# Kernel tuning notes

Measured on AMD Instinct MI355X. Metric: run time of the kernel, lower is better.

## Reference

```python
import jax, jax.numpy as jnp
import numpy as np

N_NODES = 131072
N_EDGES = 262144
N_GRAPHS = 4096
EMB = 300
N_LAYER = 5
N_TASKS = 1
NUM_ATOM_TYPE = 120
NUM_CHIRALITY = 3
NUM_BOND_TYPE = 6   # includes self-loop type 4
NUM_BOND_DIR = 3
SELF_LOOP_TYPE = 4
BN_EPS = 1e-5


def setup_inputs() -> dict:
    key = jax.random.key(0)
    ks = jax.random.split(key, 20)
    x = jnp.stack([
        jax.random.randint(ks[0], (N_NODES,), 0, NUM_ATOM_TYPE, dtype=jnp.int32),
        jax.random.randint(ks[1], (N_NODES,), 0, NUM_CHIRALITY, dtype=jnp.int32),
    ], axis=1)
    edge_index = jax.random.randint(ks[2], (2, N_EDGES), 0, N_NODES, dtype=jnp.int32)
    edge_attr = jnp.stack([
        jax.random.randint(ks[3], (N_EDGES,), 0, 4, dtype=jnp.int32),
        jax.random.randint(ks[4], (N_EDGES,), 0, NUM_BOND_DIR, dtype=jnp.int32),
    ], axis=1)
    # sorted batch vector, every graph non-empty (32 nodes per graph)
    batch = jnp.repeat(jnp.arange(N_GRAPHS, dtype=jnp.int32), N_NODES // N_GRAPHS)
    s = 0.05
    params = {
        'atom_emb0': jax.random.normal(ks[5], (NUM_ATOM_TYPE, EMB), jnp.float32) * s,
        'atom_emb1': jax.random.normal(ks[6], (NUM_CHIRALITY, EMB), jnp.float32) * s,
        'bond_emb0': jax.random.normal(ks[7], (N_LAYER, NUM_BOND_TYPE, EMB), jnp.float32) * s,
        'bond_emb1': jax.random.normal(ks[8], (N_LAYER, NUM_BOND_DIR, EMB), jnp.float32) * s,
        'W1': jax.random.normal(ks[9], (N_LAYER, EMB, 2 * EMB), jnp.float32) * s,
        'b1': jnp.zeros((N_LAYER, 2 * EMB), jnp.float32),
        'W2': jax.random.normal(ks[10], (N_LAYER, 2 * EMB, EMB), jnp.float32) * s,
        'b2': jnp.zeros((N_LAYER, EMB), jnp.float32),
        'bn_gamma': jnp.ones((N_LAYER, EMB), jnp.float32),
        'bn_beta': jnp.zeros((N_LAYER, EMB), jnp.float32),
        'head_W1': jax.random.normal(ks[11], (EMB, EMB // 2), jnp.float32) * s,
        'head_b1': jnp.zeros((EMB // 2,), jnp.float32),
        'head_W2': jax.random.normal(ks[12], (EMB // 2, N_TASKS), jnp.float32) * s,
        'head_b2': jnp.zeros((N_TASKS,), jnp.float32),
    }
    return dict(x=x, edge_index=edge_index, edge_attr=edge_attr, batch=batch,
                num_graphs=N_GRAPHS, **params)


def _gnn_forward(x, edge_index, edge_attr, batch, num_graphs,
                 atom_emb0, atom_emb1, bond_emb0, bond_emb1,
                 W1, b1, W2, b2, bn_gamma, bn_beta,
                 head_W1, head_b1, head_W2, head_b2):
    n = x.shape[0]
    L = W1.shape[0]
    # add self loops with bond type SELF_LOOP_TYPE
    loop = jnp.arange(n, dtype=edge_index.dtype)
    src = jnp.concatenate([edge_index[0], loop])
    dst = jnp.concatenate([edge_index[1], loop])
    ea0 = jnp.concatenate([edge_attr[:, 0], jnp.full((n,), SELF_LOOP_TYPE, edge_attr.dtype)])
    ea1 = jnp.concatenate([edge_attr[:, 1], jnp.zeros((n,), edge_attr.dtype)])

    h = atom_emb0[x[:, 0]] + atom_emb1[x[:, 1]]  # [N, EMB]
    for l in range(L):
        e = bond_emb0[l][ea0] + bond_emb1[l][ea1]           # [E+N, EMB]
        msg = h[src] + e                                     # gather + add
        agg = jax.ops.segment_sum(msg, dst, num_segments=n)  # [N, EMB]
        hid = jax.nn.relu(agg @ W1[l] + b1[l])
        h2 = hid @ W2[l] + b2[l]
        # BatchNorm1d (training-mode batch stats)
        mean = jnp.mean(h2, axis=0)
        var = jnp.var(h2, axis=0)
        h2 = (h2 - mean) * jax.lax.rsqrt(var + BN_EPS) * bn_gamma[l] + bn_beta[l]
        h = h2 if l == L - 1 else jax.nn.relu(h2)
    # super_node_rep: last node of each graph (batch is sorted)
    last_idx = jax.ops.segment_max(jnp.arange(n), batch, num_segments=num_graphs)
    sup = h[last_idx]                                        # [G, EMB]
    out = jax.nn.elu(sup @ head_W1 + head_b1) @ head_W2 + head_b2
    return out                                               # [G, num_tasks]


def reference(x, edge_index, edge_attr, batch, num_graphs,
              atom_emb0, atom_emb1, bond_emb0, bond_emb1,
              W1, b1, W2, b2, bn_gamma, bn_beta,
              head_W1, head_b1, head_W2, head_b2):
    return _gnn_forward(x, edge_index, edge_attr, batch, num_graphs,
                        atom_emb0, atom_emb1, bond_emb0, bond_emb1,
                        W1, b1, W2, b2, bn_gamma, bn_beta,
                        head_W1, head_b1, head_W2, head_b2)
```

## Files before the change

kernel.cpp:

```cpp
#include <hip/hip_runtime.h>
#include <hip/hip_bf16.h>

#define NN 131072
#define NE 262144
#define NG 4096
#define EMB 300
#define HS 320
#define K1 320
#define N1 640
#define K2E 608
#define N2P 384
#define NLAYER 5
#define NRB (NN / 128)

typedef __attribute__((ext_vector_type(8))) short short8;
typedef __attribute__((ext_vector_type(4))) float f32x4;
typedef __attribute__((ext_vector_type(4))) unsigned short ushort4v;

__device__ __forceinline__ void gload_lds16(const void* g, void* l) {
  __builtin_amdgcn_global_load_lds((const __attribute__((address_space(1))) void*)g,
                                   (__attribute__((address_space(3))) void*)l, 16, 0, 0);
}
__device__ __forceinline__ float b2f(unsigned short u) {
  return __uint_as_float(((unsigned)u) << 16);
}
__device__ __forceinline__ unsigned short f2b(float x) {
  __hip_bfloat16 b = __float2bfloat16(x);
  return *(unsigned short*)&b;
}


__global__ void prep_w1(const float* __restrict__ W1, __hip_bfloat16* __restrict__ W1T) {
  int idx = blockIdx.x * 256 + threadIdx.x;
  if (idx >= NLAYER * N1 * K1) return;
  int l = idx / (N1 * K1); int r = idx % (N1 * K1);
  int n = r / K1; int k = r % K1;
  float v = (n < 600 && k < 300) ? W1[(size_t)(l * 300 + k) * 600 + n] : 0.f;
  W1T[idx] = __float2bfloat16(v);
}

__global__ void prep_w2(const float* __restrict__ W2, __hip_bfloat16* __restrict__ W2T) {
  int idx = blockIdx.x * 256 + threadIdx.x;
  if (idx >= NLAYER * N2P * N1) return;
  int l = idx / (N2P * N1); int r = idx % (N2P * N1);
  int n = r / N1; int k = r % N1;
  float v = (n < 300 && k < 600) ? W2[(size_t)(l * 600 + k) * 300 + n] : 0.f;
  W2T[idx] = __float2bfloat16(v);
}

__global__ void prep_bias(const float* __restrict__ b1, const float* __restrict__ b2,
                          float* __restrict__ b1p, float* __restrict__ b2p) {
  int idx = blockIdx.x * 256 + threadIdx.x;
  if (idx < NLAYER * N1) {
    int l = idx / N1, n = idx % N1;
    b1p[idx] = (n < 600) ? b1[l * 600 + n] : 0.f;
  } else {
    int k = idx - NLAYER * N1;
    if (k < NLAYER * N2P) {
      int l = k / N2P, n = k % N2P;
      b2p[k] = (n < 300) ? b2[l * 300 + n] : 0.f;
    }
  }
}

__global__ void prep_etab(const float* __restrict__ bond0, const float* __restrict__ bond1,
                          float* __restrict__ etabg) {
  int idx = blockIdx.x * 256 + threadIdx.x;
  if (idx >= NLAYER * 13 * HS) return;
  int l = idx / (13 * HS); int r = idx % (13 * HS);
  int c = r / HS; int ch = r % HS;
  float val = 0.f;
  if (ch < EMB) {
    int t0 = (c < 12) ? (c / 3) : 4;
    int t1 = (c < 12) ? (c % 3) : 0;
    val = bond0[(size_t)(l * 6 + t0) * EMB + ch] + bond1[(size_t)(l * 3 + t1) * EMB + ch];
  }
  etabg[idx] = val;
}

__global__ void init_h(const int* __restrict__ x, const float* __restrict__ ae0,
                       const float* __restrict__ ae1, __hip_bfloat16* __restrict__ h) {
  int v = blockIdx.x; int t = threadIdx.x;
  int x0 = x[2 * v], x1 = x[2 * v + 1];
  for (int c = t; c < HS; c += 256)
    h[(size_t)v * HS + c] = __float2bfloat16(c < EMB ? ae0[x0 * EMB + c] + ae1[x1 * EMB + c] : 0.f);
}


__global__ void count_edges(const int* __restrict__ ei, int* __restrict__ counts) {
  int j = blockIdx.x * 256 + threadIdx.x;
  if (j >= NE) return;
  atomicAdd(&counts[ei[NE + j]], 1);
}

__global__ void scan_block(const int* __restrict__ counts, int* __restrict__ indptr,
                           int* __restrict__ blockSums) {
  __shared__ int s[256];
  int b = blockIdx.x, t = threadIdx.x;
  int base = b * 1024 + t * 4;
  int4 c = *(const int4*)&counts[base];
  int tsum = c.x + c.y + c.z + c.w;
  s[t] = tsum;
  __syncthreads();
  for (int off = 1; off < 256; off <<= 1) {
    int v = (t >= off) ? s[t - off] : 0;
    __syncthreads();
    s[t] += v;
    __syncthreads();
  }
  int excl = (t == 0) ? 0 : s[t - 1];
  indptr[base + 0] = excl;
  indptr[base + 1] = excl + c.x;
  indptr[base + 2] = excl + c.x + c.y;
  indptr[base + 3] = excl + c.x + c.y + c.z;
  if (t == 255) blockSums[b] = s[255];
}

__global__ void scan_top(const int* __restrict__ blockSums, int* __restrict__ blockOff) {
  __shared__ int s[128];
  int t = threadIdx.x;
  s[t] = blockSums[t];
  __syncthreads();
  for (int off = 1; off < 128; off <<= 1) {
    int v = (t >= off) ? s[t - off] : 0;
    __syncthreads();
    s[t] += v;
    __syncthreads();
  }
  blockOff[t] = (t == 0) ? 0 : s[t - 1];
}

__global__ void scan_add(int* __restrict__ indptr, const int* __restrict__ blockOff) {
  int b = blockIdx.x, t = threadIdx.x;
  int off = blockOff[b];
  int base = b * 1024 + t * 4;
  indptr[base + 0] += off; indptr[base + 1] += off;
  indptr[base + 2] += off; indptr[base + 3] += off;
  if (b == 127 && t == 255) indptr[NN] = NE;
}

__global__ void scatter_edges(const int* __restrict__ ei, const int* __restrict__ ea,
                              int* __restrict__ cursor, int* __restrict__ epacked) {
  int j = blockIdx.x * 256 + threadIdx.x;
  if (j >= NE) return;
  int dst = ei[NE + j];
  int src = ei[j];
  int c = ea[2 * j] * 3 + ea[2 * j + 1];
  int pos = atomicAdd(&cursor[dst], 1);
  epacked[pos] = src | (c << 17);
}

__global__ void last_idx_kernel(const int* __restrict__ batch, int* __restrict__ lastidx) {
  int i = blockIdx.x * 256 + threadIdx.x;
  if (i >= NN) return;
  int b = batch[i];
  if (i == NN - 1 || batch[i + 1] != b) lastidx[b] = i;
}

template<int BN>
__global__ __launch_bounds__(1024)
void aggregate_kernel(const __hip_bfloat16* __restrict__ hg, const int* __restrict__ indptr,
                      const int* __restrict__ epacked, const float* __restrict__ etabg,
                      const float* __restrict__ bnsc, const float* __restrict__ bnsh,
                      __hip_bfloat16* __restrict__ agg) {
  __shared__ float etab[13 * HS];
  const int tid = threadIdx.x;
#pragma unroll
  for (int idx = tid; idx < 13 * HS; idx += 1024)
    etab[idx] = etabg[idx];
  __syncthreads();
  const int wid = tid >> 6, lane = tid & 63;
  const int cA = lane * 4, cB = 256 + lane;
  const unsigned short* h = (const unsigned short*)hg;

  f32x4 scA = {1.f, 1.f, 1.f, 1.f}, shA = {0.f, 0.f, 0.f, 0.f};
  float scB = 1.f, shB = 0.f;
  if (BN) {
    scA = *(const f32x4*)&bnsc[cA]; shA = *(const f32x4*)&bnsh[cA];
    scB = bnsc[cB]; shB = bnsh[cB];
  }
  auto trA = [&](float x, int k) -> float {
    if (BN) x = fmaxf(fmaf(x, scA[k], shA[k]), 0.f);
    return x;
  };
  auto trB = [&](float x) -> float {
    if (BN) x = fmaxf(fmaf(x, scB, shB), 0.f);
    return x;
  };
  const float* es = etab + 12 * HS;

  for (int it = 0; it < 4; ++it) {
    const int v = blockIdx.x * 64 + it * 16 + wid;
    const unsigned short* hv = h + (size_t)v * HS;
    ushort4v pA = *(const ushort4v*)(hv + cA);
    unsigned short pB = hv[cB];
    float a0 = trA(b2f(pA[0]), 0) + es[cA];
    float a1 = trA(b2f(pA[1]), 1) + es[cA + 1];
    float a2 = trA(b2f(pA[2]), 2) + es[cA + 2];
    float a3 = trA(b2f(pA[3]), 3) + es[cA + 3];
    float a4 = trB(b2f(pB)) + es[cB];

    const int jb = indptr[v], je = indptr[v + 1];
    int j = jb;
    for (; j + 2 <= je; j += 2) {
      int p0 = epacked[j], p1 = epacked[j + 1];
      const unsigned short* h0 = h + (size_t)(p0 & (NN - 1)) * HS;
      const unsigned short* h1 = h + (size_t)(p1 & (NN - 1)) * HS;
      ushort4v q0 = *(const ushort4v*)(h0 + cA);
      ushort4v q1 = *(const ushort4v*)(h1 + cA);
      unsigned short r0 = h0[cB], r1 = h1[cB];
      const float* e0 = etab + (p0 >> 17) * HS;
      const float* e1 = etab + (p1 >> 17) * HS;
      a0 += trA(b2f(q0[0]), 0) + e0[cA]     + trA(b2f(q1[0]), 0) + e1[cA];
      a1 += trA(b2f(q0[1]), 1) + e0[cA + 1] + trA(b2f(q1[1]), 1) + e1[cA + 1];
      a2 += trA(b2f(q0[2]), 2) + e0[cA + 2] + trA(b2f(q1[2]), 2) + e1[cA + 2];
      a3 += trA(b2f(q0[3]), 3) + e0[cA + 3] + trA(b2f(q1[3]), 3) + e1[cA + 3];
      a4 += trB(b2f(r0)) + e0[cB] + trB(b2f(r1)) + e1[cB];
    }
    if (j < je) {
      int p0 = epacked[j];
      const unsigned short* h0 = h + (size_t)(p0 & (NN - 1)) * HS;
      ushort4v q0 = *(const ushort4v*)(h0 + cA);
      unsigned short r0 = h0[cB];
      const float* e0 = etab + (p0 >> 17) * HS;
      a0 += trA(b2f(q0[0]), 0) + e0[cA];
      a1 += trA(b2f(q0[1]), 1) + e0[cA + 1];
      a2 += trA(b2f(q0[2]), 2) + e0[cA + 2];
      a3 += trA(b2f(q0[3]), 3) + e0[cA + 3];
      a4 += trB(b2f(r0)) + e0[cB];
    }

    unsigned short* av = (unsigned short*)agg + (size_t)v * HS;
    ushort4v o; o[0] = f2b(a0); o[1] = f2b(a1); o[2] = f2b(a2); o[3] = f2b(a3);
    *(ushort4v*)(av + cA) = o;
    av[cB] = f2b(a4);
  }
}

template<int RELU, int STATS, int NBN, int KSTRIDE, int KEXT>
__global__ __launch_bounds__(256)
void gemm_kernel(const short* __restrict__ A, const short* __restrict__ BT,
                 const float* __restrict__ bias, __hip_bfloat16* __restrict__ Cout,
                 float* __restrict__ part, int outStride, int outBound, int rbBase) {
  __shared__ short smem[3 * 8192];
  __shared__ float sred[STATS ? 128 : 1][2];
  const int tid = threadIdx.x;
  const int wid = tid >> 6, lane = tid & 63;
  const int wm = wid >> 1, wn = wid & 1;
  f32x4 acc[4][4] = {};

  const int cpx = gridDim.x >> 3;
  const int logical = (blockIdx.x & 7) * cpx + (blockIdx.x >> 3);
  const int bn = logical % NBN;
  const int bm = logical / NBN;

  const short* Ag = A + (size_t)bm * 128 * KSTRIDE;
  const short* Bg = BT + (size_t)bn * 128 * KSTRIDE;
  const int r2 = tid >> 2;
  const int ksw = ((tid & 3) ^ ((tid >> 3) & 3)) * 8;
  const int arow_h = lane & 15;
  const int koffR = (((lane >> 4) ^ ((arow_h >> 1) & 3)) * 8);

  const short* Ao = Ag + (size_t)r2 * KSTRIDE + ksw;
  const short* Bo = Bg + (size_t)r2 * KSTRIDE + ksw;

  auto stage = [&](int buf, int kt) {
    short* s = smem + buf * 8192;
    gload_lds16(Ao + kt,                 s + tid * 8);
    gload_lds16(Ao + kt + 64 * KSTRIDE,  s + 2048 + tid * 8);
    gload_lds16(Bo + kt,                 s + 4096 + tid * 8);
    gload_lds16(Bo + kt + 64 * KSTRIDE,  s + 6144 + tid * 8);
  };

  constexpr int NT = KEXT / 32;
  stage(0, 0);
  stage(1, 32);
#pragma unroll
  for (int t = 0; t < NT; ++t) {
    if (t + 1 < NT) asm volatile("s_waitcnt vmcnt(4)" ::: "memory");
    else            asm volatile("s_waitcnt vmcnt(0)" ::: "memory");
    __builtin_amdgcn_sched_barrier(0);
    __builtin_amdgcn_s_barrier();
    const int rb = t % 3;
    if (t + 2 < NT) stage((t + 2) % 3, (t + 2) * 32);
    const short* sA = smem + rb * 8192 + wm * 2048;
    const short* sB = smem + rb * 8192 + 4096 + wn * 2048;
    short8 af[4], bf[4];
#pragma unroll
    for (int i = 0; i < 4; i++) af[i] = *(const short8*)&sA[(arow_h + i * 16) * 32 + koffR];
#pragma unroll
    for (int j = 0; j < 4; j++) bf[j] = *(const short8*)&sB[(arow_h + j * 16) * 32 + koffR];
#pragma unroll
    for (int i = 0; i < 4; i++)
#pragma unroll
      for (int j = 0; j < 4; j++)
        acc[i][j] = __builtin_amdgcn_mfma_f32_16x16x32_bf16(af[i], bf[j], acc[i][j], 0, 0, 0);
    __builtin_amdgcn_sched_barrier(0);
  }

  const int row0 = bm * 128 + wm * 64 + (lane >> 4) * 4;
  const int col0 = bn * 128 + wn * 64 + (lane & 15);
  float bs[4];
#pragma unroll
  for (int j = 0; j < 4; j++) bs[j] = bias[col0 + j * 16];
  float ssum[4] = {0, 0, 0, 0}, ssq[4] = {0, 0, 0, 0};
  if (STATS) {
    if (tid < 128) { sred[tid][0] = 0.f; sred[tid][1] = 0.f; }
    __syncthreads();
  }
#pragma unroll
  for (int i = 0; i < 4; i++) {
#pragma unroll
    for (int p = 0; p < 4; p++) {
      const size_t row = row0 + i * 16 + p;
#pragma unroll
      for (int j = 0; j < 4; j++) {
        const int col = col0 + j * 16;
        float v = acc[i][j][p] + bs[j];
        if (STATS) { ssum[j] += v; ssq[j] += v * v; }
        if (RELU) v = fmaxf(v, 0.f);
        if (col < outBound)
          Cout[row * (size_t)outStride + col] = __float2bfloat16(v);
      }
    }
  }
  if (STATS) {
#pragma unroll
    for (int j = 0; j < 4; j++) {
      const int cw = wn * 64 + j * 16 + (lane & 15);
      atomicAdd(&sred[cw][0], ssum[j]);
      atomicAdd(&sred[cw][1], ssq[j]);
    }
    __syncthreads();
    if (tid < 128) {
      const int col = bn * 128 + tid;
      if (col < EMB) {
        const int rb2 = rbBase + bm;
        part[(size_t)col * (2 * NRB) + rb2] = sred[tid][0];
        part[(size_t)col * (2 * NRB) + NRB + rb2] = sred[tid][1];
      }
    }
  }
}

__global__ __launch_bounds__(256)
void bn_finalize(const float* __restrict__ part, const float* __restrict__ gamma,
                 const float* __restrict__ beta, float* __restrict__ bnsc,
                 float* __restrict__ bnsh) {
  __shared__ float rs[256], rq[256];
  const int c = blockIdx.x, t = threadIdx.x;
  if (c >= EMB) {
    if (t == 0) { bnsc[c] = 0.f; bnsh[c] = 0.f; }
    return;
  }
  float s = 0.f, q = 0.f;
  for (int rb = t; rb < NRB; rb += 256) {
    s += part[(size_t)c * (2 * NRB) + rb];
    q += part[(size_t)c * (2 * NRB) + NRB + rb];
  }
  rs[t] = s; rq[t] = q;
  __syncthreads();
  for (int off = 128; off > 0; off >>= 1) {
    if (t < off) { rs[t] += rs[t + off]; rq[t] += rq[t + off]; }
    __syncthreads();
  }
  if (t == 0) {
    float mean = rs[0] / (float)NN;
    float var = rq[0] / (float)NN - mean * mean;
    float sc = rsqrtf(var + 1e-5f) * gamma[c];
    bnsc[c] = sc;
    bnsh[c] = beta[c] - mean * sc;
  }
}

__global__ __launch_bounds__(256)
void head_kernel(const __hip_bfloat16* __restrict__ h, const int* __restrict__ lastidx,
                 const float* __restrict__ bnsc4, const float* __restrict__ bnsh4,
                 const float* __restrict__ hW1, const float* __restrict__ hb1,
                 const float* __restrict__ hW2, const float* __restrict__ hb2,
                 float* __restrict__ out) {
  __shared__ float sup[EMB];
  __shared__ float red[256];
  int g = blockIdx.x, t = threadIdx.x;
  int v = lastidx[g];
  for (int c = t; c < EMB; c += 256)
    sup[c] = b2f(((const unsigned short*)h)[(size_t)v * HS + c]) * bnsc4[c] + bnsh4[c];
  __syncthreads();
  float val = 0.f;
  if (t < 150) {
    float acc = hb1[t];
    for (int k = 0; k < EMB; k++) acc += sup[k] * hW1[k * 150 + t];
    float e = (acc > 0.f) ? acc : (expf(acc) - 1.f);
    val = e * hW2[t];
  }
  red[t] = val;
  __syncthreads();
  for (int off = 128; off > 0; off >>= 1) {
    if (t < off) red[t] += red[t + off];
    __syncthreads();
  }
  if (t == 0) out[g] = red[0] + hb2[0];
}


extern "C" void kernel_launch(void* const* d_in, const int* in_sizes, int n_in,
                              void* d_out, int out_size, void* d_ws, size_t ws_size,
                              hipStream_t stream) {
  const int* x      = (const int*)d_in[0];
  const int* ei     = (const int*)d_in[1];
  const int* ea     = (const int*)d_in[2];
  const int* batch  = (const int*)d_in[3];
  const float* atom0 = (const float*)d_in[5];
  const float* atom1 = (const float*)d_in[6];
  const float* bond0 = (const float*)d_in[7];
  const float* bond1 = (const float*)d_in[8];
  const float* W1    = (const float*)d_in[9];
  const float* b1    = (const float*)d_in[10];
  const float* W2    = (const float*)d_in[11];
  const float* b2    = (const float*)d_in[12];
  const float* gamma = (const float*)d_in[13];
  const float* beta  = (const float*)d_in[14];
  const float* hW1   = (const float*)d_in[15];
  const float* hb1   = (const float*)d_in[16];
  const float* hW2   = (const float*)d_in[17];
  const float* hb2   = (const float*)d_in[18];
  float* out = (float*)d_out;

  char* p = (char*)d_ws;
  auto carve = [&](size_t b) -> void* {
    void* r = (void*)p;
    p += (b + 255) & ~(size_t)255;
    return r;
  };
  __hip_bfloat16* agg = (__hip_bfloat16*)carve((size_t)NN * HS * 2);
  __hip_bfloat16* h   = (__hip_bfloat16*)carve((size_t)NN * HS * 2);
  __hip_bfloat16* W1T = (__hip_bfloat16*)carve((size_t)NLAYER * N1 * K1 * 2);
  __hip_bfloat16* W2T = (__hip_bfloat16*)carve((size_t)NLAYER * N2P * N1 * 2);
  float* b1p          = (float*)carve((size_t)NLAYER * N1 * 4);
  float* b2p          = (float*)carve((size_t)NLAYER * N2P * 4);
  float* etabg        = (float*)carve((size_t)NLAYER * 13 * HS * 4);
  float* part         = (float*)carve((size_t)EMB * 2 * NRB * 4);
  float* bnsc         = (float*)carve((size_t)NLAYER * HS * 4);
  float* bnsh         = (float*)carve((size_t)NLAYER * HS * 4);
  int* counts         = (int*)carve((size_t)NN * 4);
  int* indptr         = (int*)carve((size_t)(NN + 1) * 4);
  int* cursor         = (int*)carve((size_t)NN * 4);
  int* epacked        = (int*)carve((size_t)NE * 4);
  int* blockSums      = (int*)carve(128 * 4);
  int* blockOff       = (int*)carve(128 * 4);
  int* lastidx        = (int*)carve((size_t)NG * 4);

  size_t used = (size_t)(p - (char*)d_ws);
  size_t avail = (ws_size > used + 4096) ? (ws_size - used - 4096) : 0;
  int CHUNK = 16384;
  if (avail >= (size_t)65536 * N1 * 2) CHUNK = 65536;
  else if (avail >= (size_t)32768 * N1 * 2) CHUNK = 32768;
  __hip_bfloat16* hid = (__hip_bfloat16*)carve((size_t)CHUNK * N1 * 2);

  hipMemsetAsync(counts, 0, (size_t)NN * 4, stream);

  prep_w1<<<(NLAYER * N1 * K1 + 255) / 256, 256, 0, stream>>>(W1, W1T);
  prep_w2<<<(NLAYER * N2P * N1 + 255) / 256, 256, 0, stream>>>(W2, W2T);
  prep_bias<<<(NLAYER * (N1 + N2P) + 255) / 256, 256, 0, stream>>>(b1, b2, b1p, b2p);
  prep_etab<<<(NLAYER * 13 * HS + 255) / 256, 256, 0, stream>>>(bond0, bond1, etabg);
  init_h<<<NN, 256, 0, stream>>>(x, atom0, atom1, h);

  count_edges<<<NE / 256, 256, 0, stream>>>(ei, counts);
  scan_block<<<128, 256, 0, stream>>>(counts, indptr, blockSums);
  scan_top<<<1, 128, 0, stream>>>(blockSums, blockOff);
  scan_add<<<128, 256, 0, stream>>>(indptr, blockOff);
  hipMemcpyAsync(cursor, indptr, (size_t)NN * 4, hipMemcpyDeviceToDevice, stream);
  scatter_edges<<<NE / 256, 256, 0, stream>>>(ei, ea, cursor, epacked);
  last_idx_kernel<<<NN / 256, 256, 0, stream>>>(batch, lastidx);

  for (int l = 0; l < NLAYER; l++) {
    if (l == 0)
      aggregate_kernel<0><<<NN / 64, 1024, 0, stream>>>(
          h, indptr, epacked, etabg + (size_t)l * 13 * HS, nullptr, nullptr, agg);
    else
      aggregate_kernel<1><<<NN / 64, 1024, 0, stream>>>(
          h, indptr, epacked, etabg + (size_t)l * 13 * HS,
          bnsc + (size_t)(l - 1) * HS, bnsh + (size_t)(l - 1) * HS, agg);
    for (int c0 = 0; c0 < NN; c0 += CHUNK) {
      gemm_kernel<1, 0, N1 / 128, K1, K1><<<(CHUNK / 128) * (N1 / 128), 256, 0, stream>>>(
          (const short*)(agg + (size_t)c0 * HS),
          (const short*)(W1T + (size_t)l * N1 * K1), b1p + l * N1,
          hid, nullptr, N1, N1, 0);
      gemm_kernel<0, 1, N2P / 128, N1, K2E><<<(CHUNK / 128) * (N2P / 128), 256, 0, stream>>>(
          (const short*)hid,
          (const short*)(W2T + (size_t)l * N2P * N1), b2p + l * N2P,
          h + (size_t)c0 * HS, part, HS, HS, c0 / 128);
    }
    bn_finalize<<<HS, 256, 0, stream>>>(part, gamma + (size_t)l * EMB, beta + (size_t)l * EMB,
                                        bnsc + (size_t)l * HS, bnsh + (size_t)l * HS);
  }

  head_kernel<<<NG, 256, 0, stream>>>(h, lastidx, bnsc + 4 * HS, bnsh + 4 * HS,
                                      hW1, hb1, hW2, hb2, out);
}
```

Before: 1.655 ms.

## Process two M-tiles per GEMM block with a continuous cross-tile load pipeline

Each GEMM workgroup now computes CH=2 consecutive 128-row output tiles for the same column tile. The triple-buffered global-to-LDS prefetch runs across the tile boundary, so loads for the next tile overlap the previous tile's epilogue and the pipeline prologue is paid once per block. The grid shrinks by half, and the BN stats reduction now uses explicit barriers per tile. In exchange there are fewer blocks, which may lower occupancy or load balance, and the epilogue is serialized with the next tile's compute.

```diff
diff --git a/kernel.cpp b/kernel.cpp
--- a/kernel.cpp
+++ b/kernel.cpp
@@ -12,6 +12,7 @@
 #define N2P 384
 #define NLAYER 5
 #define NRB (NN / 128)
+#define CH 2
 
 typedef __attribute__((ext_vector_type(8))) short short8;
 typedef __attribute__((ext_vector_type(4))) float f32x4;
@@ -247,14 +248,13 @@
   const int tid = threadIdx.x;
   const int wid = tid >> 6, lane = tid & 63;
   const int wm = wid >> 1, wn = wid & 1;
-  f32x4 acc[4][4] = {};
 
   const int cpx = gridDim.x >> 3;
   const int logical = (blockIdx.x & 7) * cpx + (blockIdx.x >> 3);
   const int bn = logical % NBN;
-  const int bm = logical / NBN;
-
-  const short* Ag = A + (size_t)bm * 128 * KSTRIDE;
+  const int chain = logical / NBN;
+
+  const short* Ag = A + (size_t)(chain * CH) * 128 * KSTRIDE;
   const short* Bg = BT + (size_t)bn * 128 * KSTRIDE;
   const int r2 = tid >> 2;
   const int ksw = ((tid & 3) ^ ((tid >> 3) & 3)) * 8;
@@ -264,81 +264,93 @@
   const short* Ao = Ag + (size_t)r2 * KSTRIDE + ksw;
   const short* Bo = Bg + (size_t)r2 * KSTRIDE + ksw;
 
-  auto stage = [&](int buf, int kt) {
-    short* s = smem + buf * 8192;
-    gload_lds16(Ao + kt,                 s + tid * 8);
-    gload_lds16(Ao + kt + 64 * KSTRIDE,  s + 2048 + tid * 8);
-    gload_lds16(Bo + kt,                 s + 4096 + tid * 8);
-    gload_lds16(Bo + kt + 64 * KSTRIDE,  s + 6144 + tid * 8);
+  constexpr int NT = KEXT / 32;
+  constexpr int GT = NT * CH;
+
+  auto stage = [&](int g) {
+    const int mt = g / NT;
+    const int kt = (g % NT) * 32;
+    short* s = smem + (g % 3) * 8192;
+    gload_lds16(Ao + mt * 128 * KSTRIDE + kt,                s + tid * 8);
+    gload_lds16(Ao + mt * 128 * KSTRIDE + kt + 64 * KSTRIDE, s + 2048 + tid * 8);
+    gload_lds16(Bo + kt,                                     s + 4096 + tid * 8);
+    gload_lds16(Bo + kt + 64 * KSTRIDE,                      s + 6144 + tid * 8);
   };
 
-  constexpr int NT = KEXT / 32;
-  stage(0, 0);
-  stage(1, 32);
-#pragma unroll
-  for (int t = 0; t < NT; ++t) {
-    if (t + 1 < NT) asm volatile("s_waitcnt vmcnt(4)" ::: "memory");
-    else            asm volatile("s_waitcnt vmcnt(0)" ::: "memory");
-    __builtin_amdgcn_sched_barrier(0);
-    __builtin_amdgcn_s_barrier();
-    const int rb = t % 3;
-    if (t + 2 < NT) stage((t + 2) % 3, (t + 2) * 32);
-    const short* sA = smem + rb * 8192 + wm * 2048;
-    const short* sB = smem + rb * 8192 + 4096 + wn * 2048;
-    short8 af[4], bf[4];
-#pragma unroll
-    for (int i = 0; i < 4; i++) af[i] = *(const short8*)&sA[(arow_h + i * 16) * 32 + koffR];
-#pragma unroll
-    for (int j = 0; j < 4; j++) bf[j] = *(const short8*)&sB[(arow_h + j * 16) * 32 + koffR];
-#pragma unroll
-    for (int i = 0; i < 4; i++)
-#pragma unroll
-      for (int j = 0; j < 4; j++)
-        acc[i][j] = __builtin_amdgcn_mfma_f32_16x16x32_bf16(af[i], bf[j], acc[i][j], 0, 0, 0);
-    __builtin_amdgcn_sched_barrier(0);
-  }
-
-  const int row0 = bm * 128 + wm * 64 + (lane >> 4) * 4;
   const int col0 = bn * 128 + wn * 64 + (lane & 15);
   float bs[4];
 #pragma unroll
   for (int j = 0; j < 4; j++) bs[j] = bias[col0 + j * 16];
-  float ssum[4] = {0, 0, 0, 0}, ssq[4] = {0, 0, 0, 0};
-  if (STATS) {
-    if (tid < 128) { sred[tid][0] = 0.f; sred[tid][1] = 0.f; }
-    __syncthreads();
-  }
-#pragma unroll
-  for (int i = 0; i < 4; i++) {
-#pragma unroll
-    for (int p = 0; p < 4; p++) {
-      const size_t row = row0 + i * 16 + p;
+
+  stage(0);
+  stage(1);
+#pragma unroll
+  for (int mt = 0; mt < CH; ++mt) {
+    f32x4 acc[4][4] = {};
+#pragma unroll
+    for (int k = 0; k < NT; ++k) {
+      const int g = mt * NT + k;
+      if (g + 1 < GT) asm volatile("s_waitcnt vmcnt(4)" ::: "memory");
+      else            asm volatile("s_waitcnt vmcnt(0)" ::: "memory");
+      __builtin_amdgcn_sched_barrier(0);
+      __builtin_amdgcn_s_barrier();
+      if (g + 2 < GT) stage(g + 2);
+      const short* sA = smem + (g % 3) * 8192 + wm * 2048;
+      const short* sB = smem + (g % 3) * 8192 + 4096 + wn * 2048;
+      short8 af[4], bf[4];
+#pragma unroll
+      for (int i = 0; i < 4; i++) af[i] = *(const short8*)&sA[(arow_h + i * 16) * 32 + koffR];
+#pragma unroll
+      for (int j = 0; j < 4; j++) bf[j] = *(const short8*)&sB[(arow_h + j * 16) * 32 + koffR];
+#pragma unroll
+      for (int i = 0; i < 4; i++)
+#pragma unroll
+        for (int j = 0; j < 4; j++)
+          acc[i][j] = __builtin_amdgcn_mfma_f32_16x16x32_bf16(af[i], bf[j], acc[i][j], 0, 0, 0);
+      __builtin_amdgcn_sched_barrier(0);
+    }
+
+    const int bm = chain * CH + mt;
+    const int row0 = bm * 128 + wm * 64 + (lane >> 4) * 4;
+    float ssum[4] = {0, 0, 0, 0}, ssq[4] = {0, 0, 0, 0};
+    if (STATS) {
+      if (tid < 128) { sred[tid][0] = 0.f; sred[tid][1] = 0.f; }
+      asm volatile("s_waitcnt lgkmcnt(0)" ::: "memory");
+      __builtin_amdgcn_s_barrier();
+    }
+#pragma unroll
+    for (int i = 0; i < 4; i++) {
+#pragma unroll
+      for (int p = 0; p < 4; p++) {
+        const size_t row = row0 + i * 16 + p;
+#pragma unroll
+        for (int j = 0; j < 4; j++) {
+          const int col = col0 + j * 16;
+          float v = acc[i][j][p] + bs[j];
+          if (STATS) { ssum[j] += v; ssq[j] += v * v; }
+          if (RELU) v = fmaxf(v, 0.f);
+          if (col < outBound)
+            Cout[row * (size_t)outStride + col] = __float2bfloat16(v);
+        }
+      }
+    }
+    if (STATS) {
 #pragma unroll
       for (int j = 0; j < 4; j++) {
-        const int col = col0 + j * 16;
-        float v = acc[i][j][p] + bs[j];
-        if (STATS) { ssum[j] += v; ssq[j] += v * v; }
-        if (RELU) v = fmaxf(v, 0.f);
-        if (col < outBound)
-          Cout[row * (size_t)outStride + col] = __float2bfloat16(v);
+        const int cw = wn * 64 + j * 16 + (lane & 15);
+        atomicAdd(&sred[cw][0], ssum[j]);
+        atomicAdd(&sred[cw][1], ssq[j]);
       }
-    }
-  }
-  if (STATS) {
-#pragma unroll
-    for (int j = 0; j < 4; j++) {
-      const int cw = wn * 64 + j * 16 + (lane & 15);
-      atomicAdd(&sred[cw][0], ssum[j]);
-      atomicAdd(&sred[cw][1], ssq[j]);
-    }
-    __syncthreads();
-    if (tid < 128) {
-      const int col = bn * 128 + tid;
-      if (col < EMB) {
-        const int rb2 = rbBase + bm;
-        part[(size_t)col * (2 * NRB) + rb2] = sred[tid][0];
-        part[(size_t)col * (2 * NRB) + NRB + rb2] = sred[tid][1];
+      asm volatile("s_waitcnt lgkmcnt(0)" ::: "memory");
+      __builtin_amdgcn_s_barrier();
+      if (tid < 128) {
+        const int col = bn * 128 + tid;
+        if (col < EMB) {
+          part[(size_t)col * (2 * NRB) + rbBase + bm] = sred[tid][0];
+          part[(size_t)col * (2 * NRB) + NRB + rbBase + bm] = sred[tid][1];
+        }
       }
+      __builtin_amdgcn_s_barrier();
     }
   }
 }
@@ -482,11 +494,11 @@
           h, indptr, epacked, etabg + (size_t)l * 13 * HS,
           bnsc + (size_t)(l - 1) * HS, bnsh + (size_t)(l - 1) * HS, agg);
     for (int c0 = 0; c0 < NN; c0 += CHUNK) {
-      gemm_kernel<1, 0, N1 / 128, K1, K1><<<(CHUNK / 128) * (N1 / 128), 256, 0, stream>>>(
+      gemm_kernel<1, 0, N1 / 128, K1, K1><<<(CHUNK / (128 * CH)) * (N1 / 128), 256, 0, stream>>>(
           (const short*)(agg + (size_t)c0 * HS),
           (const short*)(W1T + (size_t)l * N1 * K1), b1p + l * N1,
           hid, nullptr, N1, N1, 0);
-      gemm_kernel<0, 1, N2P / 128, N1, K2E><<<(CHUNK / 128) * (N2P / 128), 256, 0, stream>>>(
+      gemm_kernel<0, 1, N2P / 128, N1, K2E><<<(CHUNK / (128 * CH)) * (N2P / 128), 256, 0, stream>>>(
           (const short*)hid,
           (const short*)(W2T + (size_t)l * N2P * N1), b2p + l * N2P,
           h + (size_t)c0 * HS, part, HS, HS, c0 / 128);
```

New measurement: 1.907 ms. 1.15x slower.
